# Kernel optimization log

Measured on AMD Instinct MI355X. Metric: run time of the kernel, lower is better.

The kernel has to match this reference:

```python
import jax, jax.numpy as jnp
import numpy as np

B, L, D, H = 1, 4096, 1024, 16
HD = D // H  # head dim = 64
WINDOW = 15


def _rope(t, cos, sin):
    # t: [B,H,L,HD]; cos/sin: [1,1,L,HD//2]
    tr = t.reshape(*t.shape[:-1], HD // 2, 2)
    a, b = tr[..., 0], tr[..., 1]
    out_r = a * cos - b * sin
    out_i = a * sin + b * cos
    return jnp.stack([out_r, out_i], axis=-1).reshape(t.shape)


def _longformer_mask(L, window):
    i = jnp.arange(L)[:, None]
    j = jnp.arange(L)[None, :]
    causal = j <= i
    win = jnp.abs(i - j) <= window // 2
    glob = (j == 0) | (i == 0)
    return (causal & win) | glob  # [L,L] bool


def setup_inputs() -> dict:
    key = jax.random.key(0)
    kx, kq, kk, kv, ko = jax.random.split(key, 5)
    x = jax.random.normal(kx, (B, L, D), dtype=jnp.float32)
    scale = 0.02
    Wq = jax.random.normal(kq, (D, D), dtype=jnp.float32) * scale
    Wk = jax.random.normal(kk, (D, D), dtype=jnp.float32) * scale
    Wv = jax.random.normal(kv, (D, D), dtype=jnp.float32) * scale
    Wo = jax.random.normal(ko, (D, D), dtype=jnp.float32) * scale
    # real RoPE frequencies (complex freqs_cis split into cos/sin)
    inv_freq = 1.0 / (10000.0 ** (np.arange(0, HD, 2, dtype=np.float32) / HD))
    pos = np.arange(L, dtype=np.float32)
    ang = pos[:, None] * inv_freq[None, :]  # [L, HD//2]
    freqs_cos = jnp.asarray(np.cos(ang))[None]  # [1,L,HD//2]
    freqs_sin = jnp.asarray(np.sin(ang))[None]
    return {"x": x, "Wq": Wq, "Wk": Wk, "Wv": Wv, "Wo": Wo,
            "freqs_cos": freqs_cos, "freqs_sin": freqs_sin}


def reference(x, Wq, Wk, Wv, Wo, freqs_cos, freqs_sin):
    b, l, _ = x.shape
    # projections (nn.Linear: y = x @ W^T)
    Q = (x @ Wq.T).reshape(b, l, H, HD).transpose(0, 2, 1, 3)  # [B,H,L,HD]
    K = (x @ Wk.T).reshape(b, l, H, HD).transpose(0, 2, 1, 3)
    V = (x @ Wv.T).reshape(b, l, H, HD).transpose(0, 2, 1, 3)
    cos = freqs_cos[:, None, :l]  # [1,1,L,HD//2] (torch unsqueeze(1))
    sin = freqs_sin[:, None, :l]
    Q = _rope(Q, cos, sin)
    K = _rope(K, cos, sin)
    mask = _longformer_mask(l, WINDOW)  # [L,L]
    scores = jnp.einsum('bhqd,bhkd->bhqk', Q, K) / jnp.sqrt(jnp.float32(HD))
    scores = jnp.where(mask[None, None], scores, jnp.finfo(scores.dtype).min)
    attn = jax.nn.softmax(scores, axis=-1)
    out = jnp.einsum('bhqk,bhkd->bhqd', attn, V)  # [B,H,L,HD]
    out = out.transpose(0, 2, 1, 3).reshape(b, l, D)
    return out @ Wo.T
```

## Files before the change

kernel.cpp:

```cpp
#include <hip/hip_runtime.h>
#include <stdint.h>

#define SL 4096
#define DM 1024
#define NH 16
#define HDIM 64

typedef short short8 __attribute__((ext_vector_type(8)));
typedef float f32x4 __attribute__((ext_vector_type(4)));

__device__ __forceinline__ unsigned short f2bf(float f) {
  unsigned int u = __float_as_uint(f);
  u += 0x7FFF + ((u >> 16) & 1);
  return (unsigned short)(u >> 16);
}
__device__ __forceinline__ float bf2f(unsigned short u) {
  return __uint_as_float((unsigned int)u << 16);
}
__device__ __forceinline__ float bflo(unsigned int u) { return __uint_as_float(u << 16); }
__device__ __forceinline__ float bfhi(unsigned int u) { return __uint_as_float(u & 0xffff0000u); }

__device__ __forceinline__ void gload_lds16(const void* g, void* l) {
  __builtin_amdgcn_global_load_lds((const __attribute__((address_space(1))) void*)g,
                                   (__attribute__((address_space(3))) void*)l, 16, 0, 0);
}

__global__ void cast4(const float* __restrict__ src, unsigned short* __restrict__ dst, int n4) {
  int i = blockIdx.x * blockDim.x + threadIdx.x;
  if (i >= n4) return;
  float4 v = ((const float4*)src)[i];
  ushort4 o = make_ushort4(f2bf(v.x), f2bf(v.y), f2bf(v.z), f2bf(v.w));
  ((ushort4*)dst)[i] = o;
}

__global__ void cast_weights(const float* __restrict__ Wq, const float* __restrict__ Wk,
                             const float* __restrict__ Wv, const float* __restrict__ Wo,
                             unsigned short* __restrict__ w3b, unsigned short* __restrict__ wob) {
  int i = blockIdx.x * blockDim.x + threadIdx.x;
  int seg = i >> 18;
  int off = i & 262143;
  const float* src = (seg == 0) ? Wq : (seg == 1) ? Wk : (seg == 2) ? Wv : Wo;
  unsigned short* dst = (seg < 3) ? (w3b + (size_t)seg * DM * DM) : wob;
  float4 v = ((const float4*)src)[off];
  ushort4 o = make_ushort4(f2bf(v.x), f2bf(v.y), f2bf(v.z), f2bf(v.w));
  ((ushort4*)dst)[off] = o;
}

template <bool BF16OUT, bool ROPE>
__global__ void gemm_bt(const unsigned short* __restrict__ A,
                        const unsigned short* __restrict__ B,
                        void* __restrict__ Cv,
                        int M, int N, int K, int ldc,
                        const float* __restrict__ fc, const float* __restrict__ fs) {
  __shared__ __align__(16) unsigned short As[2][128 * 32];
  __shared__ __align__(16) unsigned short Bs[2][128 * 32];
  const int tid  = threadIdx.x;
  const int w    = tid >> 6;
  const int lane = tid & 63;
  const int wr = w >> 1, wc = w & 1;
  const int brow = blockIdx.y * 128;
  const int bcol = blockIdx.x * 128;
  const int l4 = lane >> 2;
  const int lk = (lane & 3) * 8;
  const int lhalf = lane >> 4;
  const int lrow  = lane & 15;
  const int c0 = w * 2;

  const unsigned short* Ag0 = A + (size_t)(brow + c0 * 16 + l4) * K + lk;
  const unsigned short* Ag1 = A + (size_t)(brow + (c0 + 1) * 16 + l4) * K + lk;
  const unsigned short* Bg0 = B + (size_t)(bcol + c0 * 16 + l4) * K + lk;
  const unsigned short* Bg1 = B + (size_t)(bcol + (c0 + 1) * 16 + l4) * K + lk;

  f32x4 acc[4][4] = {};
  const int NT = K >> 5;

  auto STAGE = [&](int t, int b) {
    const int k0 = t << 5;
    gload_lds16(Ag0 + k0, &As[b][c0 * 512]);
    gload_lds16(Ag1 + k0, &As[b][(c0 + 1) * 512]);
    gload_lds16(Bg0 + k0, &Bs[b][c0 * 512]);
    gload_lds16(Bg1 + k0, &Bs[b][(c0 + 1) * 512]);
  };

  STAGE(0, 0);
  for (int t = 0; t < NT; ++t) {
    const int cur = t & 1;
    __syncthreads();
    if (t + 1 < NT) STAGE(t + 1, cur ^ 1);
    short8 af[4], bf[4];
#pragma unroll
    for (int m = 0; m < 4; ++m)
      af[m] = *(const short8*)&As[cur][(wr * 64 + m * 16 + lrow) * 32 + lhalf * 8];
#pragma unroll
    for (int n = 0; n < 4; ++n)
      bf[n] = *(const short8*)&Bs[cur][(wc * 64 + n * 16 + lrow) * 32 + lhalf * 8];
#pragma unroll
    for (int m = 0; m < 4; ++m)
#pragma unroll
      for (int n = 0; n < 4; ++n)
        acc[m][n] = __builtin_amdgcn_mfma_f32_16x16x32_bf16(af[m], bf[n], acc[m][n], 0, 0, 0);
  }

  const int er = (lane >> 4) * 4;
  const int ec = lane & 15;

  if constexpr (ROPE) {
    if (bcol + wc * 64 < 2048) {
#pragma unroll
      for (int n = 0; n < 4; ++n) {
        const int p = ((n * 16 + ec) & 63) >> 1;
#pragma unroll
        for (int m = 0; m < 4; ++m) {
#pragma unroll
          for (int r = 0; r < 4; ++r) {
            const int row = brow + wr * 64 + m * 16 + er + r;
            float v = acc[m][n][r];
            float pv = __shfl_xor(v, 1);
            float cs = fc[row * 32 + p], sn = fs[row * 32 + p];
            acc[m][n][r] = (lane & 1) ? (pv * sn + v * cs) : (v * cs - pv * sn);
          }
        }
      }
    }
  }

#pragma unroll
  for (int m = 0; m < 4; ++m)
#pragma unroll
    for (int n = 0; n < 4; ++n) {
      const size_t roff = (size_t)(brow + wr * 64 + m * 16 + er) * ldc + (bcol + wc * 64 + n * 16 + ec);
      if constexpr (BF16OUT) {
        unsigned short* cp = (unsigned short*)Cv + roff;
#pragma unroll
        for (int r = 0; r < 4; ++r) cp[(size_t)r * ldc] = f2bf(acc[m][n][r]);
      } else {
        float* cp = (float*)Cv + roff;
#pragma unroll
        for (int r = 0; r < 4; ++r) cp[(size_t)r * ldc] = acc[m][n][r];
      }
    }
}

__global__ __launch_bounds__(64)
void attn_row0_part(const unsigned short* __restrict__ qkv, float* __restrict__ prt) {
  const int p = blockIdx.x;
  const int h = blockIdx.y;
  const int lane = threadIdx.x;
  const float q = bf2f(qkv[h * 64 + lane]);
  float m = -1e30f, s = 0.f, o = 0.f;
  const int j0 = p * 32;
  for (int jj = 0; jj < 32; ++jj) {
    const int j = j0 + jj;
    float kv = bf2f(qkv[(size_t)j * 3072 + 1024 + h * 64 + lane]);
    float pr = q * kv;
#pragma unroll
    for (int off = 32; off; off >>= 1) pr += __shfl_xor(pr, off);
    pr *= 0.125f;
    float mn = fmaxf(m, pr);
    float c = __expf(m - mn);
    float e = __expf(pr - mn);
    float v = bf2f(qkv[(size_t)j * 3072 + 2048 + h * 64 + lane]);
    s = s * c + e;
    o = o * c + e * v;
    m = mn;
  }
  float* dst = prt + ((size_t)h * 128 + p) * 72;
  if (lane == 0) { dst[0] = m; dst[1] = s; }
  dst[2 + lane] = o;
}

__global__ __launch_bounds__(64)
void attn_row0_combine(const float* __restrict__ prt, unsigned short* __restrict__ atb) {
  const int h = blockIdx.x;
  const int lane = threadIdx.x;
  const float* base = prt + (size_t)h * 128 * 72;
  __shared__ float cbuf[128];
  float m0 = base[lane * 72];
  float m1 = base[(lane + 64) * 72];
  float M = fmaxf(m0, m1);
#pragma unroll
  for (int off = 32; off; off >>= 1) M = fmaxf(M, __shfl_xor(M, off));
  float c0 = __expf(m0 - M), c1 = __expf(m1 - M);
  float ls = base[lane * 72 + 1] * c0 + base[(lane + 64) * 72 + 1] * c1;
#pragma unroll
  for (int off = 32; off; off >>= 1) ls += __shfl_xor(ls, off);
  cbuf[lane] = c0;
  cbuf[lane + 64] = c1;
  __syncthreads();
  float o = 0.f;
#pragma unroll 8
  for (int p = 0; p < 128; ++p) o += cbuf[p] * base[p * 72 + 2 + lane];
  atb[h * 64 + lane] = f2bf(o / ls);
}

__global__ __launch_bounds__(256)
void attn_main(const unsigned short* __restrict__ qkv, unsigned short* __restrict__ atb) {
  const int i = blockIdx.x * 4 + (threadIdx.x >> 6) + 1;
  if (i >= SL) return;
  const int lane = threadIdx.x & 63;
  const unsigned short* rowQ = qkv + (size_t)i * 3072 + lane * 16;

  float q[16];
  {
    uint4 a = *(const uint4*)rowQ;
    uint4 b = *(const uint4*)(rowQ + 8);
    unsigned int uu[8] = {a.x, a.y, a.z, a.w, b.x, b.y, b.z, b.w};
#pragma unroll
    for (int c = 0; c < 8; ++c) { q[2 * c] = bflo(uu[c]); q[2 * c + 1] = bfhi(uu[c]); }
  }

  float sc[9];
#pragma unroll
  for (int t = 0; t < 9; ++t) {
    int j = (t == 0) ? 0 : (i - 8 + t);
    bool valid = (t == 0) || (j >= 1);
    int jc = valid ? j : 0;
    const unsigned short* pk = qkv + (size_t)jc * 3072 + 1024 + lane * 16;
    uint4 a = *(const uint4*)pk;
    uint4 b = *(const uint4*)(pk + 8);
    unsigned int uu[8] = {a.x, a.y, a.z, a.w, b.x, b.y, b.z, b.w};
    float pr = 0.f;
#pragma unroll
    for (int c = 0; c < 8; ++c) pr += bflo(uu[c]) * q[2 * c] + bfhi(uu[c]) * q[2 * c + 1];
    pr += __shfl_xor(pr, 1);
    pr += __shfl_xor(pr, 2);
    sc[t] = valid ? pr * 0.125f : -1e30f;
  }

  float mx = sc[0];
#pragma unroll
  for (int t = 1; t < 9; ++t) mx = fmaxf(mx, sc[t]);
  float s = 0.f;
#pragma unroll
  for (int t = 0; t < 9; ++t) { float e = __expf(sc[t] - mx); sc[t] = e; s += e; }
  const float inv = 1.0f / s;

  float o[16] = {};
#pragma unroll
  for (int t = 0; t < 9; ++t) {
    int j = (t == 0) ? 0 : (i - 8 + t);
    bool valid = (t == 0) || (j >= 1);
    int jc = valid ? j : 0;
    const unsigned short* pv = qkv + (size_t)jc * 3072 + 2048 + lane * 16;
    uint4 a = *(const uint4*)pv;
    uint4 b = *(const uint4*)(pv + 8);
    unsigned int uu[8] = {a.x, a.y, a.z, a.w, b.x, b.y, b.z, b.w};
#pragma unroll
    for (int c = 0; c < 8; ++c) {
      o[2 * c]     += sc[t] * bflo(uu[c]);
      o[2 * c + 1] += sc[t] * bfhi(uu[c]);
    }
  }

  unsigned int wv[8];
#pragma unroll
  for (int c = 0; c < 8; ++c)
    wv[c] = (unsigned int)f2bf(o[2 * c] * inv) | ((unsigned int)f2bf(o[2 * c + 1] * inv) << 16);
  unsigned short* po = atb + (size_t)i * 1024 + lane * 16;
  uint4 s0; s0.x = wv[0]; s0.y = wv[1]; s0.z = wv[2]; s0.w = wv[3];
  uint4 s1; s1.x = wv[4]; s1.y = wv[5]; s1.z = wv[6]; s1.w = wv[7];
  *(uint4*)po = s0;
  *(uint4*)(po + 8) = s1;
}

extern "C" void kernel_launch(void* const* d_in, const int* in_sizes, int n_in,
                              void* d_out, int out_size, void* d_ws, size_t ws_size,
                              hipStream_t stream) {
  const float* x  = (const float*)d_in[0];
  const float* Wq = (const float*)d_in[1];
  const float* Wk = (const float*)d_in[2];
  const float* Wv = (const float*)d_in[3];
  const float* Wo = (const float*)d_in[4];
  const float* fc = (const float*)d_in[5];
  const float* fs = (const float*)d_in[6];
  float* out = (float*)d_out;

  char* ws = (char*)d_ws;
  unsigned short* xb   = (unsigned short*)(ws);
  unsigned short* w3b  = (unsigned short*)(ws + ((size_t)8 << 20));
  unsigned short* wob  = (unsigned short*)(ws + ((size_t)14 << 20));
  unsigned short* qkvb = (unsigned short*)(ws + ((size_t)16 << 20));
  unsigned short* atb  = (unsigned short*)(ws + ((size_t)40 << 20));
  float*          prt  = (float*)(ws + ((size_t)48 << 20));

  cast4<<<(SL * DM / 4 + 255) / 256, 256, 0, stream>>>(x, xb, SL * DM / 4);
  cast_weights<<<(4 * DM * DM / 4) / 256, 256, 0, stream>>>(Wq, Wk, Wv, Wo, w3b, wob);

  dim3 g1(3072 / 128, SL / 128);
  gemm_bt<true, true><<<g1, 256, 0, stream>>>(xb, w3b, (void*)qkvb, SL, 3072, DM, 3072, fc, fs);

  attn_row0_part<<<dim3(128, NH), 64, 0, stream>>>(qkvb, prt);
  attn_row0_combine<<<NH, 64, 0, stream>>>(prt, atb);
  attn_main<<<1024, 256, 0, stream>>>(qkvb, atb);

  dim3 g2(DM / 128, SL / 128);
  gemm_bt<false, false><<<g2, 256, 0, stream>>>(atb, wob, (void*)out, SL, DM, DM, DM, nullptr, nullptr);
}
```

Before: 104.4 us.

## Fuse cast and attention kernels, enlarge QKV GEMM tile, swizzle LDS and block order

```diff
diff --git a/kernel.cpp b/kernel.cpp
--- a/kernel.cpp
+++ b/kernel.cpp
@@ -25,61 +25,89 @@
                                    (__attribute__((address_space(3))) void*)l, 16, 0, 0);
 }
 
-__global__ void cast4(const float* __restrict__ src, unsigned short* __restrict__ dst, int n4) {
+__global__ void cast_all(const float* __restrict__ x,
+                         const float* __restrict__ Wq, const float* __restrict__ Wk,
+                         const float* __restrict__ Wv, const float* __restrict__ Wo,
+                         unsigned short* __restrict__ xb,
+                         unsigned short* __restrict__ w3b, unsigned short* __restrict__ wob) {
   int i = blockIdx.x * blockDim.x + threadIdx.x;
-  if (i >= n4) return;
-  float4 v = ((const float4*)src)[i];
-  ushort4 o = make_ushort4(f2bf(v.x), f2bf(v.y), f2bf(v.z), f2bf(v.w));
-  ((ushort4*)dst)[i] = o;
-}
-
-__global__ void cast_weights(const float* __restrict__ Wq, const float* __restrict__ Wk,
-                             const float* __restrict__ Wv, const float* __restrict__ Wo,
-                             unsigned short* __restrict__ w3b, unsigned short* __restrict__ wob) {
-  int i = blockIdx.x * blockDim.x + threadIdx.x;
-  int seg = i >> 18;
-  int off = i & 262143;
-  const float* src = (seg == 0) ? Wq : (seg == 1) ? Wk : (seg == 2) ? Wv : Wo;
-  unsigned short* dst = (seg < 3) ? (w3b + (size_t)seg * DM * DM) : wob;
+  const float* src;
+  unsigned short* dst;
+  int off;
+  if (i < (1 << 20)) {
+    src = x; dst = xb; off = i;
+  } else {
+    int wsel = i - (1 << 20);
+    int seg = wsel >> 18;
+    off = wsel & 262143;
+    src = (seg == 0) ? Wq : (seg == 1) ? Wk : (seg == 2) ? Wv : Wo;
+    dst = (seg < 3) ? (w3b + (size_t)seg * DM * DM) : wob;
+  }
   float4 v = ((const float4*)src)[off];
   ushort4 o = make_ushort4(f2bf(v.x), f2bf(v.y), f2bf(v.z), f2bf(v.w));
   ((ushort4*)dst)[off] = o;
 }
 
-template <bool BF16OUT, bool ROPE>
+template <int BM, int BN, bool BF16OUT, bool ROPE>
 __global__ void gemm_bt(const unsigned short* __restrict__ A,
                         const unsigned short* __restrict__ B,
                         void* __restrict__ Cv,
                         int M, int N, int K, int ldc,
                         const float* __restrict__ fc, const float* __restrict__ fs) {
-  __shared__ __align__(16) unsigned short As[2][128 * 32];
-  __shared__ __align__(16) unsigned short Bs[2][128 * 32];
+  constexpr int WM = BM / 64, WN = BN / 64, W = WM * WN;
+  constexpr int ACW = BM / 16 / W;
+  constexpr int BCW = BN / 16 / W;
+  __shared__ __align__(16) unsigned short As[2][BM * 32];
+  __shared__ __align__(16) unsigned short Bs[2][BN * 32];
   const int tid  = threadIdx.x;
   const int w    = tid >> 6;
   const int lane = tid & 63;
-  const int wr = w >> 1, wc = w & 1;
-  const int brow = blockIdx.y * 128;
-  const int bcol = blockIdx.x * 128;
+  const int wr = w / WN, wc = w % WN;
+
+  const int gx = gridDim.x;
+  const int total = gx * gridDim.y;
+  const int lin = blockIdx.y * gx + blockIdx.x;
+  const int swz = (lin & 7) * (total >> 3) + (lin >> 3);
+  const int brow = (swz / gx) * BM;
+  const int bcol = (swz % gx) * BN;
+
   const int l4 = lane >> 2;
-  const int lk = (lane & 3) * 8;
-  const int lhalf = lane >> 4;
-  const int lrow  = lane & 15;
-  const int c0 = w * 2;
-
-  const unsigned short* Ag0 = A + (size_t)(brow + c0 * 16 + l4) * K + lk;
-  const unsigned short* Ag1 = A + (size_t)(brow + (c0 + 1) * 16 + l4) * K + lk;
-  const unsigned short* Bg0 = B + (size_t)(bcol + c0 * 16 + l4) * K + lk;
-  const unsigned short* Bg1 = B + (size_t)(bcol + (c0 + 1) * 16 + l4) * K + lk;
+  const int lkS = (((lane & 3) ^ ((lane >> 3) & 3))) * 8;
+  const int lrow = lane & 15;
+  const int sw8 = (((lane >> 4) ^ ((lane >> 1) & 3))) * 8;
+
+  const unsigned short* Ag[ACW];
+  const unsigned short* Bg[BCW];
+#pragma unroll
+  for (int c = 0; c < ACW; ++c)
+    Ag[c] = A + (size_t)(brow + (w * ACW + c) * 16 + l4) * K + lkS;
+#pragma unroll
+  for (int c = 0; c < BCW; ++c)
+    Bg[c] = B + (size_t)(bcol + (w * BCW + c) * 16 + l4) * K + lkS;
 
   f32x4 acc[4][4] = {};
   const int NT = K >> 5;
 
   auto STAGE = [&](int t, int b) {
     const int k0 = t << 5;
-    gload_lds16(Ag0 + k0, &As[b][c0 * 512]);
-    gload_lds16(Ag1 + k0, &As[b][(c0 + 1) * 512]);
-    gload_lds16(Bg0 + k0, &Bs[b][c0 * 512]);
-    gload_lds16(Bg1 + k0, &Bs[b][(c0 + 1) * 512]);
+#pragma unroll
+    for (int c = 0; c < ACW; ++c) gload_lds16(Ag[c] + k0, &As[b][(w * ACW + c) * 512]);
+#pragma unroll
+    for (int c = 0; c < BCW; ++c) gload_lds16(Bg[c] + k0, &Bs[b][(w * BCW + c) * 512]);
+  };
+  auto COMPUTE = [&](int cur) {
+    short8 af[4], bf[4];
+#pragma unroll
+    for (int m = 0; m < 4; ++m)
+      af[m] = *(const short8*)&As[cur][(wr * 64 + m * 16 + lrow) * 32 + sw8];
+#pragma unroll
+    for (int n = 0; n < 4; ++n)
+      bf[n] = *(const short8*)&Bs[cur][(wc * 64 + n * 16 + lrow) * 32 + sw8];
+#pragma unroll
+    for (int m = 0; m < 4; ++m)
+#pragma unroll
+      for (int n = 0; n < 4; ++n)
+        acc[m][n] = __builtin_amdgcn_mfma_f32_16x16x32_bf16(af[m], bf[n], acc[m][n], 0, 0, 0);
   };
 
   STAGE(0, 0);
@@ -87,18 +115,7 @@
     const int cur = t & 1;
     __syncthreads();
     if (t + 1 < NT) STAGE(t + 1, cur ^ 1);
-    short8 af[4], bf[4];
-#pragma unroll
-    for (int m = 0; m < 4; ++m)
-      af[m] = *(const short8*)&As[cur][(wr * 64 + m * 16 + lrow) * 32 + lhalf * 8];
-#pragma unroll
-    for (int n = 0; n < 4; ++n)
-      bf[n] = *(const short8*)&Bs[cur][(wc * 64 + n * 16 + lrow) * 32 + lhalf * 8];
-#pragma unroll
-    for (int m = 0; m < 4; ++m)
-#pragma unroll
-      for (int n = 0; n < 4; ++n)
-        acc[m][n] = __builtin_amdgcn_mfma_f32_16x16x32_bf16(af[m], bf[n], acc[m][n], 0, 0, 0);
+    COMPUTE(cur);
   }
 
   const int er = (lane >> 4) * 4;
@@ -141,32 +158,103 @@
     }
 }
 
-__global__ __launch_bounds__(64)
-void attn_row0_part(const unsigned short* __restrict__ qkv, float* __restrict__ prt) {
-  const int p = blockIdx.x;
-  const int h = blockIdx.y;
-  const int lane = threadIdx.x;
-  const float q = bf2f(qkv[h * 64 + lane]);
-  float m = -1e30f, s = 0.f, o = 0.f;
-  const int j0 = p * 32;
-  for (int jj = 0; jj < 32; ++jj) {
-    const int j = j0 + jj;
-    float kv = bf2f(qkv[(size_t)j * 3072 + 1024 + h * 64 + lane]);
-    float pr = q * kv;
-#pragma unroll
-    for (int off = 32; off; off >>= 1) pr += __shfl_xor(pr, off);
-    pr *= 0.125f;
-    float mn = fmaxf(m, pr);
-    float c = __expf(m - mn);
-    float e = __expf(pr - mn);
-    float v = bf2f(qkv[(size_t)j * 3072 + 2048 + h * 64 + lane]);
-    s = s * c + e;
-    o = o * c + e * v;
-    m = mn;
-  }
-  float* dst = prt + ((size_t)h * 128 + p) * 72;
-  if (lane == 0) { dst[0] = m; dst[1] = s; }
-  dst[2 + lane] = o;
+__global__ __launch_bounds__(256)
+void attn_fused(const unsigned short* __restrict__ qkv, unsigned short* __restrict__ atb,
+                float* __restrict__ prt) {
+  const int wid = threadIdx.x >> 6;
+  const int lane = threadIdx.x & 63;
+  if (blockIdx.x >= 1024) {
+    const int u = (blockIdx.x - 1024) * 4 + wid;
+    const int p = u & 127, h = u >> 7;
+    const float q = bf2f(qkv[h * 64 + lane]);
+    float m = -1e30f, s = 0.f, o = 0.f;
+    const int j0 = p * 32;
+    for (int jj = 0; jj < 32; ++jj) {
+      const int j = j0 + jj;
+      float kv = bf2f(qkv[(size_t)j * 3072 + 1024 + h * 64 + lane]);
+      float pr = q * kv;
+#pragma unroll
+      for (int off = 32; off; off >>= 1) pr += __shfl_xor(pr, off);
+      pr *= 0.125f;
+      float mn = fmaxf(m, pr);
+      float c = __expf(m - mn);
+      float e = __expf(pr - mn);
+      float v = bf2f(qkv[(size_t)j * 3072 + 2048 + h * 64 + lane]);
+      s = s * c + e;
+      o = o * c + e * v;
+      m = mn;
+    }
+    float* dst = prt + ((size_t)h * 128 + p) * 72;
+    if (lane == 0) { dst[0] = m; dst[1] = s; }
+    dst[2 + lane] = o;
+    return;
+  }
+
+  const int i = blockIdx.x * 4 + wid + 1;
+  if (i >= SL) return;
+  const unsigned short* rowQ = qkv + (size_t)i * 3072 + lane * 16;
+
+  float q[16];
+  {
+    uint4 a = *(const uint4*)rowQ;
+    uint4 b = *(const uint4*)(rowQ + 8);
+    unsigned int uu[8] = {a.x, a.y, a.z, a.w, b.x, b.y, b.z, b.w};
+#pragma unroll
+    for (int c = 0; c < 8; ++c) { q[2 * c] = bflo(uu[c]); q[2 * c + 1] = bfhi(uu[c]); }
+  }
+
+  float sc[9];
+#pragma unroll
+  for (int t = 0; t < 9; ++t) {
+    int j = (t == 0) ? 0 : (i - 8 + t);
+    bool valid = (t == 0) || (j >= 1);
+    int jc = valid ? j : 0;
+    const unsigned short* pk = qkv + (size_t)jc * 3072 + 1024 + lane * 16;
+    uint4 a = *(const uint4*)pk;
+    uint4 b = *(const uint4*)(pk + 8);
+    unsigned int uu[8] = {a.x, a.y, a.z, a.w, b.x, b.y, b.z, b.w};
+    float pr = 0.f;
+#pragma unroll
+    for (int c = 0; c < 8; ++c) pr += bflo(uu[c]) * q[2 * c] + bfhi(uu[c]) * q[2 * c + 1];
+    pr += __shfl_xor(pr, 1);
+    pr += __shfl_xor(pr, 2);
+    sc[t] = valid ? pr * 0.125f : -1e30f;
+  }
+
+  float mx = sc[0];
+#pragma unroll
+  for (int t = 1; t < 9; ++t) mx = fmaxf(mx, sc[t]);
+  float s = 0.f;
+#pragma unroll
+  for (int t = 0; t < 9; ++t) { float e = __expf(sc[t] - mx); sc[t] = e; s += e; }
+  const float inv = 1.0f / s;
+
+  float o[16] = {};
+#pragma unroll
+  for (int t = 0; t < 9; ++t) {
+    int j = (t == 0) ? 0 : (i - 8 + t);
+    bool valid = (t == 0) || (j >= 1);
+    int jc = valid ? j : 0;
+    const unsigned short* pv = qkv + (size_t)jc * 3072 + 2048 + lane * 16;
+    uint4 a = *(const uint4*)pv;
+    uint4 b = *(const uint4*)(pv + 8);
+    unsigned int uu[8] = {a.x, a.y, a.z, a.w, b.x, b.y, b.z, b.w};
+#pragma unroll
+    for (int c = 0; c < 8; ++c) {
+      o[2 * c]     += sc[t] * bflo(uu[c]);
+      o[2 * c + 1] += sc[t] * bfhi(uu[c]);
+    }
+  }
+
+  unsigned int wv[8];
+#pragma unroll
+  for (int c = 0; c < 8; ++c)
+    wv[c] = (unsigned int)f2bf(o[2 * c] * inv) | ((unsigned int)f2bf(o[2 * c + 1] * inv) << 16);
+  unsigned short* po = atb + (size_t)i * 1024 + lane * 16;
+  uint4 s0; s0.x = wv[0]; s0.y = wv[1]; s0.z = wv[2]; s0.w = wv[3];
+  uint4 s1; s1.x = wv[4]; s1.y = wv[5]; s1.z = wv[6]; s1.w = wv[7];
+  *(uint4*)po = s0;
+  *(uint4*)(po + 8) = s1;
 }
 
 __global__ __launch_bounds__(64)
@@ -191,76 +279,6 @@
 #pragma unroll 8
   for (int p = 0; p < 128; ++p) o += cbuf[p] * base[p * 72 + 2 + lane];
   atb[h * 64 + lane] = f2bf(o / ls);
-}
-
-__global__ __launch_bounds__(256)
-void attn_main(const unsigned short* __restrict__ qkv, unsigned short* __restrict__ atb) {
-  const int i = blockIdx.x * 4 + (threadIdx.x >> 6) + 1;
-  if (i >= SL) return;
-  const int lane = threadIdx.x & 63;
-  const unsigned short* rowQ = qkv + (size_t)i * 3072 + lane * 16;
-
-  float q[16];
-  {
-    uint4 a = *(const uint4*)rowQ;
-    uint4 b = *(const uint4*)(rowQ + 8);
-    unsigned int uu[8] = {a.x, a.y, a.z, a.w, b.x, b.y, b.z, b.w};
-#pragma unroll
-    for (int c = 0; c < 8; ++c) { q[2 * c] = bflo(uu[c]); q[2 * c + 1] = bfhi(uu[c]); }
-  }
-
-  float sc[9];
-#pragma unroll
-  for (int t = 0; t < 9; ++t) {
-    int j = (t == 0) ? 0 : (i - 8 + t);
-    bool valid = (t == 0) || (j >= 1);
-    int jc = valid ? j : 0;
-    const unsigned short* pk = qkv + (size_t)jc * 3072 + 1024 + lane * 16;
-    uint4 a = *(const uint4*)pk;
-    uint4 b = *(const uint4*)(pk + 8);
-    unsigned int uu[8] = {a.x, a.y, a.z, a.w, b.x, b.y, b.z, b.w};
-    float pr = 0.f;
-#pragma unroll
-    for (int c = 0; c < 8; ++c) pr += bflo(uu[c]) * q[2 * c] + bfhi(uu[c]) * q[2 * c + 1];
-    pr += __shfl_xor(pr, 1);
-    pr += __shfl_xor(pr, 2);
-    sc[t] = valid ? pr * 0.125f : -1e30f;
-  }
-
-  float mx = sc[0];
-#pragma unroll
-  for (int t = 1; t < 9; ++t) mx = fmaxf(mx, sc[t]);
-  float s = 0.f;
-#pragma unroll
-  for (int t = 0; t < 9; ++t) { float e = __expf(sc[t] - mx); sc[t] = e; s += e; }
-  const float inv = 1.0f / s;
-
-  float o[16] = {};
-#pragma unroll
-  for (int t = 0; t < 9; ++t) {
-    int j = (t == 0) ? 0 : (i - 8 + t);
-    bool valid = (t == 0) || (j >= 1);
-    int jc = valid ? j : 0;
-    const unsigned short* pv = qkv + (size_t)jc * 3072 + 2048 + lane * 16;
-    uint4 a = *(const uint4*)pv;
-    uint4 b = *(const uint4*)(pv + 8);
-    unsigned int uu[8] = {a.x, a.y, a.z, a.w, b.x, b.y, b.z, b.w};
-#pragma unroll
-    for (int c = 0; c < 8; ++c) {
-      o[2 * c]     += sc[t] * bflo(uu[c]);
-      o[2 * c + 1] += sc[t] * bfhi(uu[c]);
-    }
-  }
-
-  unsigned int wv[8];
-#pragma unroll
-  for (int c = 0; c < 8; ++c)
-    wv[c] = (unsigned int)f2bf(o[2 * c] * inv) | ((unsigned int)f2bf(o[2 * c + 1] * inv) << 16);
-  unsigned short* po = atb + (size_t)i * 1024 + lane * 16;
-  uint4 s0; s0.x = wv[0]; s0.y = wv[1]; s0.z = wv[2]; s0.w = wv[3];
-  uint4 s1; s1.x = wv[4]; s1.y = wv[5]; s1.z = wv[6]; s1.w = wv[7];
-  *(uint4*)po = s0;
-  *(uint4*)(po + 8) = s1;
 }
 
 extern "C" void kernel_launch(void* const* d_in, const int* in_sizes, int n_in,
@@ -283,16 +301,14 @@
   unsigned short* atb  = (unsigned short*)(ws + ((size_t)40 << 20));
   float*          prt  = (float*)(ws + ((size_t)48 << 20));
 
-  cast4<<<(SL * DM / 4 + 255) / 256, 256, 0, stream>>>(x, xb, SL * DM / 4);
-  cast_weights<<<(4 * DM * DM / 4) / 256, 256, 0, stream>>>(Wq, Wk, Wv, Wo, w3b, wob);
-
-  dim3 g1(3072 / 128, SL / 128);
-  gemm_bt<true, true><<<g1, 256, 0, stream>>>(xb, w3b, (void*)qkvb, SL, 3072, DM, 3072, fc, fs);
-
-  attn_row0_part<<<dim3(128, NH), 64, 0, stream>>>(qkvb, prt);
+  cast_all<<<(2 * (1 << 20)) / 256, 256, 0, stream>>>(x, Wq, Wk, Wv, Wo, xb, w3b, wob);
+
+  dim3 g1(3072 / 128, SL / 256);
+  gemm_bt<256, 128, true, true><<<g1, 512, 0, stream>>>(xb, w3b, (void*)qkvb, SL, 3072, DM, 3072, fc, fs);
+
+  attn_fused<<<1536, 256, 0, stream>>>(qkvb, atb, prt);
   attn_row0_combine<<<NH, 64, 0, stream>>>(prt, atb);
-  attn_main<<<1024, 256, 0, stream>>>(qkvb, atb);
 
   dim3 g2(DM / 128, SL / 128);
-  gemm_bt<false, false><<<g2, 256, 0, stream>>>(atb, wob, (void*)out, SL, DM, DM, DM, nullptr, nullptr);
-}
+  gemm_bt<128, 128, false, false><<<g2, 256, 0, stream>>>(atb, wob, (void*)out, SL, DM, DM, DM, nullptr, nullptr);
+}
```

After: 102.4 us. About the same (-1.9%).
